# Optimization experiments

Hardware: AMD Instinct MI355X
Metric: run time of the kernel (lower is better)

## Reference

```python
import jax, jax.numpy as jnp
import numpy as np

B = 128          # graphs
N = 512          # nodes per graph
NT = B * N       # total nodes = 65536
E = NT * 16      # total edges = 1048576
IN = 64
H = 128
OUT = 2
L = 4            # num_layers
RATIO = 0.8


def setup_inputs() -> dict:
    key = jax.random.key(0)
    ks = jax.random.split(key, 20)

    def w(k, shape, fan_in):
        return jax.random.normal(k, shape, jnp.float32) / np.sqrt(fan_in)

    x = jax.random.normal(ks[0], (NT, IN), jnp.float32)
    edge_index = jax.random.randint(ks[1], (2, E), 0, NT, dtype=jnp.int32)
    batch = (jnp.arange(NT) // N).astype(jnp.int32)  # equal-size graphs

    return {
        "x": x,
        "edge_index": edge_index,
        "batch": batch,
        # conv1: GraphConv(IN, H, aggr='mean') -> lin_rel (w/ bias) + lin_root (no bias)
        "W1_rel": w(ks[2], (IN, H), IN),
        "W1_root": w(ks[3], (IN, H), IN),
        "b1": jnp.zeros((H,), jnp.float32),
        # convs[0..2]: GraphConv(H, H, aggr='mean'), stacked
        "Wc_rel": w(ks[4], (L - 1, H, H), H),
        "Wc_root": w(ks[5], (L - 1, H, H), H),
        "bc": jnp.zeros((L - 1, H), jnp.float32),
        # SAGPooling score GNN: GraphConv(H, 1) with default aggr='add'
        "pw_rel": w(ks[6], (H,), H),
        "pw_root": w(ks[7], (H,), H),
        "pb": jnp.zeros((1,), jnp.float32),
        # MLP head
        "lin1_W": w(ks[8], (L * H, H), L * H),
        "lin1_b": jnp.zeros((H,), jnp.float32),
        "lin2_W": w(ks[9], (H, OUT), H),
        "lin2_b": jnp.zeros((OUT,), jnp.float32),
    }


def _graph_conv_mean(x, src, dst, emask, W_rel, W_root, b, n):
    # PyG GraphConv: lin_rel(mean_{j->i} x_j) + lin_root(x_i); masked edges excluded.
    msg = x[src] * emask[:, None]                                  # [E, D] gather
    s = jax.ops.segment_sum(msg, dst, num_segments=n)              # [n, D] scatter-add
    cnt = jax.ops.segment_sum(emask, dst, num_segments=n)          # [n]
    agg = s / jnp.maximum(cnt, 1.0)[:, None]                       # zero for isolated nodes
    return agg @ W_rel + x @ W_root + b


def reference(x, edge_index, batch, W1_rel, W1_root, b1, Wc_rel, Wc_root, bc,
              pw_rel, pw_root, pb, lin1_W, lin1_b, lin2_W, lin2_b):
    src = edge_index[0]
    dst = edge_index[1]
    emask = jnp.ones((E,), jnp.float32)
    n = NT
    npg = N  # nodes per graph (all graphs equal size)

    h = jax.nn.relu(_graph_conv_mean(x, src, dst, emask, W1_rel, W1_root, b1, n))
    xs = [h.reshape(B, npg, H).mean(axis=1)]  # global_mean_pool

    for i in range(L - 1):
        h = jax.nn.relu(_graph_conv_mean(h, src, dst, emask, Wc_rel[i], Wc_root[i], bc[i], n))
        xs.append(h.reshape(B, npg, H).mean(axis=1))
        if i % 2 == 0 and i < L - 2:
            # ---- SAGPooling: score via GraphConv(H,1) with add aggregation ----
            smsg = jax.ops.segment_sum(h[src] * emask[:, None], dst, num_segments=n)
            score = smsg @ pw_rel + h @ pw_root + pb[0]            # [n]
            k = int(np.ceil(RATIO * npg))
            topv, topi = jax.lax.top_k(score.reshape(B, npg), k)   # per-graph top-k
            perm = (jnp.arange(B)[:, None] * npg + topi).reshape(-1)  # global kept ids
            h = h[perm] * jnp.tanh(topv.reshape(-1))[:, None]
            # remap edges; edges touching dropped nodes get masked out
            node_map = jnp.full((n,), -1, jnp.int32).at[perm].set(
                jnp.arange(B * k, dtype=jnp.int32))
            ns, nd = node_map[src], node_map[dst]
            keep = ((ns >= 0) & (nd >= 0)).astype(jnp.float32)
            emask = emask * keep
            src = jnp.where(ns >= 0, ns, 0)
            dst = jnp.where(nd >= 0, nd, 0)
            n = B * k
            npg = k

    xcat = jnp.concatenate(xs, axis=-1)                            # JumpingKnowledge 'cat'
    out = jax.nn.relu(xcat @ lin1_W + lin1_b)
    # dropout is identity in eval mode
    out = out @ lin2_W + lin2_b
    return jax.nn.log_softmax(out, axis=-1)
```

## Files before the change

### kernel.cpp

```cpp
#include <hip/hip_runtime.h>
#include <math.h>

#define NT 65536
#define EE 1048576
#define NB 128
#define KK 410
#define HH 128

typedef short bf16x8 __attribute__((ext_vector_type(8)));
typedef float f32x4 __attribute__((ext_vector_type(4)));

__device__ unsigned short g_xb[(size_t)NT * 64];
__device__ unsigned short g_hb1[(size_t)NT * HH];
__device__ unsigned short g_hb2[(size_t)NT * HH];
__device__ unsigned short g_wt1[128 * 128];
__device__ unsigned short g_wtc[3 * 128 * 256];
__device__ unsigned short g_csr1u[EE];
__device__ unsigned short g_keptu[NT];
__device__ unsigned int g_ebuck[EE];
__device__ int g_bcnt[128];
__device__ int g_bcur[128];
__device__ float g_trel[NT];
__device__ float g_troot[NT];
__device__ float g_gatef[NT];
__device__ float g_kinv[NT];
__device__ float g_xc8[4 * NB * 8 * 128];
__device__ int g_rows1[NT + 1];

__device__ __forceinline__ unsigned short* ubuf(int id) {
    switch (id) {
        case 0: return g_xb;
        case 1: return g_hb1;
        case 2: return g_hb2;
        case 3: return g_wt1;
        case 4: return g_wtc;
    }
    return g_xb;
}

__device__ __forceinline__ float b2f(unsigned short u) {
    union { unsigned int i; float f; } v;
    v.i = ((unsigned int)u) << 16;
    return v.f;
}
__device__ __forceinline__ unsigned short f2b(float f) {
    unsigned int x = __float_as_uint(f);
    unsigned int r = x + 0x7fffu + ((x >> 16) & 1u);
    return (unsigned short)(r >> 16);
}
__device__ __forceinline__ bf16x8 scale8(bf16x8 a, float g) {
    bf16x8 r;
#pragma unroll
    for (int i = 0; i < 8; i++) {
        unsigned short u = (unsigned short)a[i];
        r[i] = (short)f2b(b2f(u) * g);
    }
    return r;
}

__global__ __launch_bounds__(256) void k_prep(const float* __restrict__ x,
                                              const float* __restrict__ W1r,
                                              const float* __restrict__ W1o,
                                              const float* __restrict__ Wcr,
                                              const float* __restrict__ Wco,
                                              const int* __restrict__ dst) {
    if (blockIdx.x < 4544) {
        int tid = blockIdx.x * 256 + threadIdx.x;
        if (tid < 1048576) {
            float4 v = *(const float4*)&x[(size_t)tid * 4];
            unsigned int lo = (unsigned int)f2b(v.x) | ((unsigned int)f2b(v.y) << 16);
            unsigned int hi = (unsigned int)f2b(v.z) | ((unsigned int)f2b(v.w) << 16);
            *(uint2*)&g_xb[(size_t)tid * 4] = make_uint2(lo, hi);
        } else if (tid < 1048576 + 16384) {
            int r = tid - 1048576;
            int k = r & 127, n = r >> 7;
            float v = (k < 64) ? W1r[k * 128 + n] : W1o[(k - 64) * 128 + n];
            g_wt1[n * 128 + k] = f2b(v);
        } else {
            int r = tid - (1048576 + 16384);
            int l = r >> 15;
            int k = r & 255, n = (r >> 8) & 127;
            float v = (k < 128) ? Wcr[l * 16384 + k * 128 + n]
                                : Wco[l * 16384 + (k - 128) * 128 + n];
            g_wtc[l * 32768 + n * 256 + k] = f2b(v);
        }
    } else {
        __shared__ int h[128];
        if (threadIdx.x < 128) h[threadIdx.x] = 0;
        __syncthreads();
        int e0 = ((blockIdx.x - 4544) * 256 + threadIdx.x) * 4;
        int4 d = *(const int4*)&dst[e0];
        atomicAdd(&h[d.x >> 9], 1);
        atomicAdd(&h[d.y >> 9], 1);
        atomicAdd(&h[d.z >> 9], 1);
        atomicAdd(&h[d.w >> 9], 1);
        __syncthreads();
        if (threadIdx.x < 128 && h[threadIdx.x]) atomicAdd(&g_bcnt[threadIdx.x], h[threadIdx.x]);
    }
}

__global__ __launch_bounds__(256) void k_bscatter(const int* __restrict__ src,
                                                  const int* __restrict__ dst) {
    __shared__ int h[128];
    __shared__ int base[128];
    __shared__ int sc[128];
    __shared__ int vv[128];
    int t = threadIdx.x;
    if (t < 128) { vv[t] = g_bcnt[t]; sc[t] = vv[t]; h[t] = 0; }
    __syncthreads();
    for (int off = 1; off < 128; off <<= 1) {
        int u = (t >= off && t < 128) ? sc[t - off] : 0;
        __syncthreads();
        if (t < 128) sc[t] += u;
        __syncthreads();
    }
    int e0 = (blockIdx.x * 256 + t) * 4;
    int4 s = *(const int4*)&src[e0];
    int4 d = *(const int4*)&dst[e0];
    int b0 = d.x >> 9, b1 = d.y >> 9, b2 = d.z >> 9, b3 = d.w >> 9;
    atomicAdd(&h[b0], 1);
    atomicAdd(&h[b1], 1);
    atomicAdd(&h[b2], 1);
    atomicAdd(&h[b3], 1);
    __syncthreads();
    if (t < 128) {
        int c = h[t];
        base[t] = (sc[t] - vv[t]) + (c ? atomicAdd(&g_bcur[t], c) : 0);
        h[t] = 0;
    }
    __syncthreads();
    int r0 = atomicAdd(&h[b0], 1);
    g_ebuck[base[b0] + r0] = ((unsigned int)(d.x & 511) << 16) | (unsigned int)s.x;
    int r1 = atomicAdd(&h[b1], 1);
    g_ebuck[base[b1] + r1] = ((unsigned int)(d.y & 511) << 16) | (unsigned int)s.y;
    int r2 = atomicAdd(&h[b2], 1);
    g_ebuck[base[b2] + r2] = ((unsigned int)(d.z & 511) << 16) | (unsigned int)s.z;
    int r3 = atomicAdd(&h[b3], 1);
    g_ebuck[base[b3] + r3] = ((unsigned int)(d.w & 511) << 16) | (unsigned int)s.w;
}

__global__ __launch_bounds__(512) void k_bcsr() {
    __shared__ int hist[512];
    __shared__ int offs[512];
    __shared__ int cur[512];
    __shared__ int sc[128];
    int g = blockIdx.x, t = threadIdx.x;
    if (t < 128) sc[t] = g_bcnt[t];
    hist[t] = 0;
    cur[t] = 0;
    __syncthreads();
    for (int off = 1; off < 128; off <<= 1) {
        int u = (t >= off && t < 128) ? sc[t - off] : 0;
        __syncthreads();
        if (t < 128) sc[t] += u;
        __syncthreads();
    }
    int b0 = sc[g] - g_bcnt[g];
    int b1 = sc[g];
    for (int e = b0 + t; e < b1; e += 512) {
        unsigned int p = g_ebuck[e];
        atomicAdd(&hist[p >> 16], 1);
    }
    __syncthreads();
    int v = hist[t];
    offs[t] = v;
    __syncthreads();
    for (int off = 1; off < 512; off <<= 1) {
        int u = (t >= off) ? offs[t - off] : 0;
        __syncthreads();
        offs[t] += u;
        __syncthreads();
    }
    int excl = offs[t] - v;
    g_rows1[g * 512 + t] = b0 + excl;
    if (t == 511) g_rows1[g * 512 + 512] = b0 + excl + v;
    __syncthreads();
    offs[t] = excl;
    __syncthreads();
    for (int e = b0 + t; e < b1; e += 512) {
        unsigned int p = g_ebuck[e];
        int dl = p >> 16;
        int r = atomicAdd(&cur[dl], 1);
        g_csr1u[b0 + offs[dl] + r] = (unsigned short)(p & 0xFFFFu);
    }
}

template <int KA, int KB, int KC, int GATED, int MASKED, int DOTS, int BGATE>
__global__ __launch_bounds__(256, 4) void k_conv(int hId, int bId, int wId, int wOfs,
                                                 const float* __restrict__ bias, int outId,
                                                 int sec,
                                                 const float* __restrict__ pwr,
                                                 const float* __restrict__ pwt) {
    constexpr int NCHA = KA / 32;
    const int K = KA + KB;
    const unsigned short* h = ubuf(hId);
    const unsigned short* Bp = ubuf(bId);
    const unsigned short* Wt = ubuf(wId) + wOfs;
    unsigned short* out = ubuf(outId);
    __shared__ float s[128];
    int lane = threadIdx.x & 63;
    int w = threadIdx.x >> 6;
    int n16 = lane & 15, quad = lane >> 4;
    int rowbase = blockIdx.x * 64;
    int rowg = rowbase + w * 16;
    int node = rowg + n16;
    if (threadIdx.x < 128) s[threadIdx.x] = 0.f;

    int r0 = g_rows1[node], r1 = g_rows1[node + 1];
    float aggacc[NCHA][8];
#pragma unroll
    for (int ch = 0; ch < NCHA; ch++)
#pragma unroll
        for (int j = 0; j < 8; j++) aggacc[ch][j] = 0.f;
    int kc = 0;
    const unsigned short* hq = h + quad * 8;
#define ACC8(arow, v, gf)                                        \
    arow[0] += gf * b2f((unsigned short)(v.x & 0xffff));         \
    arow[1] += gf * b2f((unsigned short)(v.x >> 16));            \
    arow[2] += gf * b2f((unsigned short)(v.y & 0xffff));         \
    arow[3] += gf * b2f((unsigned short)(v.y >> 16));            \
    arow[4] += gf * b2f((unsigned short)(v.z & 0xffff));         \
    arow[5] += gf * b2f((unsigned short)(v.z >> 16));            \
    arow[6] += gf * b2f((unsigned short)(v.w & 0xffff));         \
    arow[7] += gf * b2f((unsigned short)(v.w >> 16));
    int e = r0;
    for (; e + 2 <= r1; e += 2) {
        int i0 = g_csr1u[e], i1 = g_csr1u[e + 1];
        uint4 v0[NCHA], v1[NCHA];
#pragma unroll
        for (int ch = 0; ch < NCHA; ch++)
            v0[ch] = *(const uint4*)&hq[(size_t)i0 * KA + ch * 32];
#pragma unroll
        for (int ch = 0; ch < NCHA; ch++)
            v1[ch] = *(const uint4*)&hq[(size_t)i1 * KA + ch * 32];
        float gf0 = GATED ? g_gatef[i0] : 1.0f;
        float gf1 = GATED ? g_gatef[i1] : 1.0f;
        if (KC == 1) kc += (int)g_keptu[i0] + (int)g_keptu[i1];
#pragma unroll
        for (int ch = 0; ch < NCHA; ch++) { ACC8(aggacc[ch], v0[ch], gf0) }
#pragma unroll
        for (int ch = 0; ch < NCHA; ch++) { ACC8(aggacc[ch], v1[ch], gf1) }
    }
    if (e < r1) {
        int i0 = g_csr1u[e];
        uint4 v0[NCHA];
#pragma unroll
        for (int ch = 0; ch < NCHA; ch++)
            v0[ch] = *(const uint4*)&hq[(size_t)i0 * KA + ch * 32];
        float gf0 = GATED ? g_gatef[i0] : 1.0f;
        if (KC == 1) kc += (int)g_keptu[i0];
#pragma unroll
        for (int ch = 0; ch < NCHA; ch++) { ACC8(aggacc[ch], v0[ch], gf0) }
    }
#undef ACC8
    float inv;
    if (KC == 0) {
        int c = r1 - r0;
        inv = 1.0f / (float)(c > 0 ? c : 1);
    } else if (KC == 1) {
        inv = 1.0f / (float)(kc > 0 ? kc : 1);
        if (quad == 0) g_kinv[node] = inv;
    } else {
        inv = g_kinv[node];
    }

    bf16x8 afrag[NCHA];
#pragma unroll
    for (int ch = 0; ch < NCHA; ch++)
#pragma unroll
        for (int j = 0; j < 8; j++) afrag[ch][j] = (short)f2b(aggacc[ch][j] * inv);

    float ga = BGATE ? g_gatef[node] : 1.0f;
    f32x4 acc[8];
#pragma unroll
    for (int ct = 0; ct < 8; ct++)
#pragma unroll
        for (int i = 0; i < 4; i++) acc[ct][i] = 0.f;
#pragma unroll
    for (int ks = 0; ks < 8; ks++) {
        if (ks >= K / 32) break;
        bf16x8 a;
        if (ks < NCHA) {
            a = afrag[ks];
        } else {
            int kk = (ks - NCHA) * 32;
            a = *(const bf16x8*)&Bp[(size_t)node * KB + kk + quad * 8];
            if (BGATE) a = scale8(a, ga);
        }
#pragma unroll
        for (int ct = 0; ct < 8; ct++) {
            bf16x8 b = *(const bf16x8*)&Wt[(size_t)(ct * 16 + n16) * K + ks * 32 + quad * 8];
            acc[ct] = __builtin_amdgcn_mfma_f32_16x16x32_bf16(a, b, acc[ct], 0, 0, 0);
        }
    }

    {
        float m[4];
#pragma unroll
        for (int i = 0; i < 4; i++) {
            int r = rowg + quad * 4 + i;
            m[i] = (!MASKED || g_keptu[r]) ? 1.0f : 0.0f;
        }
#pragma unroll
        for (int ct = 0; ct < 8; ct++) {
            int c = ct * 16 + n16;
            float bv = bias[c];
#pragma unroll
            for (int i = 0; i < 4; i++) {
                int r = rowg + quad * 4 + i;
                float v = fmaxf(acc[ct][i] + bv, 0.f) * m[i];
                acc[ct][i] = v;
                out[(size_t)r * 128 + c] = f2b(v);
            }
        }
    }
    __syncthreads();

#pragma unroll
    for (int ct = 0; ct < 8; ct++) {
        float p = acc[ct][0] + acc[ct][1] + acc[ct][2] + acc[ct][3];
        p += __shfl_xor(p, 16);
        p += __shfl_xor(p, 32);
        if (quad == 0) atomicAdd(&s[ct * 16 + n16], p);
    }

    if (DOTS) {
        float pr[8], pt[8];
#pragma unroll
        for (int ct = 0; ct < 8; ct++) {
            pr[ct] = pwr[ct * 16 + n16];
            pt[ct] = pwt[ct * 16 + n16];
        }
#pragma unroll
        for (int i = 0; i < 4; i++) {
            float dr = 0.f, dt = 0.f;
#pragma unroll
            for (int ct = 0; ct < 8; ct++) {
                dr += acc[ct][i] * pr[ct];
                dt += acc[ct][i] * pt[ct];
            }
            dr += __shfl_xor(dr, 1); dt += __shfl_xor(dt, 1);
            dr += __shfl_xor(dr, 2); dt += __shfl_xor(dt, 2);
            dr += __shfl_xor(dr, 4); dt += __shfl_xor(dt, 4);
            dr += __shfl_xor(dr, 8); dt += __shfl_xor(dt, 8);
            if (n16 == 0) {
                int r = rowg + quad * 4 + i;
                g_trel[r] = dr;
                g_troot[r] = dt;
            }
        }
    }
    __syncthreads();
    if (threadIdx.x < 128) {
        int g = blockIdx.x >> 3, e8 = blockIdx.x & 7;
        g_xc8[((sec * NB + g) * 8 + e8) * 128 + threadIdx.x] = s[threadIdx.x];
    }
}

__global__ __launch_bounds__(256) void k_topk(const float* __restrict__ pb) {
    __shared__ float sv[512];
    __shared__ int si[512];
    int g = blockIdx.x, t = threadIdx.x;
    if (t == 0) { g_bcnt[g] = 0; g_bcur[g] = 0; }
    float pbv = pb[0];
    for (int l = t; l < 512; l += 256) {
        int node = g * 512 + l;
        int r0 = g_rows1[node], r1 = g_rows1[node + 1];
        float s = 0.f;
        int e = r0;
        for (; e + 4 <= r1; e += 4) {
            float s0 = g_trel[g_csr1u[e]];
            float s1 = g_trel[g_csr1u[e + 1]];
            float s2 = g_trel[g_csr1u[e + 2]];
            float s3 = g_trel[g_csr1u[e + 3]];
            s += (s0 + s1) + (s2 + s3);
        }
        for (; e < r1; e++) s += g_trel[g_csr1u[e]];
        sv[l] = s + g_troot[node] + pbv;
        si[l] = l;
    }
    __syncthreads();
    for (int k = 2; k <= 512; k <<= 1) {
        for (int j = k >> 1; j > 0; j >>= 1) {
            for (int i = t; i < 512; i += 256) {
                int p = i ^ j;
                if (p > i) {
                    float va = sv[i], vb = sv[p];
                    int ia = si[i], ib = si[p];
                    bool aFirst = (va > vb) || (va == vb && ia < ib);
                    bool up = ((i & k) == 0);
                    if (up != aFirst) { sv[i] = vb; sv[p] = va; si[i] = ib; si[p] = ia; }
                }
            }
            __syncthreads();
        }
    }
    for (int r = t; r < 512; r += 256) {
        int old = g * 512 + si[r];
        if (r < KK) {
            g_gatef[old] = tanhf(sv[r]);
            g_keptu[old] = 1;
        } else {
            g_gatef[old] = 0.f;
            g_keptu[old] = 0;
        }
    }
}

__global__ __launch_bounds__(128) void k_head(const float* __restrict__ W1, const float* __restrict__ b1,
                                              const float* __restrict__ W2, const float* __restrict__ b2,
                                              float* __restrict__ out) {
    __shared__ float xr[512];
    __shared__ float r0[128], r1[128];
    int g = blockIdx.x, t = threadIdx.x;
    for (int i = t; i < 512; i += 128) {
        int sec = i >> 7, c = i & 127;
        const float* p = &g_xc8[((sec * NB + g) * 8) * 128 + c];
        float v = 0.f;
#pragma unroll
        for (int q = 0; q < 8; q++) v += p[q * 128];
        float inv = (sec < 2) ? (1.0f / 512.0f) : (1.0f / 410.0f);
        xr[i] = v * inv;
    }
    __syncthreads();
    float acc = b1[t];
    for (int k = 0; k < 512; k++) acc += xr[k] * W1[k * 128 + t];
    acc = fmaxf(acc, 0.f);
    r0[t] = acc * W2[t * 2 + 0];
    r1[t] = acc * W2[t * 2 + 1];
    __syncthreads();
    for (int off = 64; off > 0; off >>= 1) {
        if (t < off) { r0[t] += r0[t + off]; r1[t] += r1[t + off]; }
        __syncthreads();
    }
    if (t == 0) {
        float z0 = r0[0] + b2[0], z1 = r1[0] + b2[1];
        float m = fmaxf(z0, z1);
        float l = m + logf(expf(z0 - m) + expf(z1 - m));
        out[g * 2 + 0] = z0 - l;
        out[g * 2 + 1] = z1 - l;
    }
}

extern "C" void kernel_launch(void* const* d_in, const int* in_sizes, int n_in,
                              void* d_out, int out_size, void* d_ws, size_t ws_size,
                              hipStream_t stream) {
    const float* x = (const float*)d_in[0];
    const int* ei = (const int*)d_in[1];
    const int* src = ei;
    const int* dst = ei + EE;
    const float* W1r = (const float*)d_in[3];
    const float* W1o = (const float*)d_in[4];
    const float* b1 = (const float*)d_in[5];
    const float* Wcr = (const float*)d_in[6];
    const float* Wco = (const float*)d_in[7];
    const float* bc = (const float*)d_in[8];
    const float* pwr = (const float*)d_in[9];
    const float* pwt = (const float*)d_in[10];
    const float* pb = (const float*)d_in[11];
    const float* l1W = (const float*)d_in[12];
    const float* l1b = (const float*)d_in[13];
    const float* l2W = (const float*)d_in[14];
    const float* l2b = (const float*)d_in[15];
    float* out = (float*)d_out;

    k_prep<<<5568, 256, 0, stream>>>(x, W1r, W1o, Wcr, Wco, dst);

    k_bscatter<<<1024, 256, 0, stream>>>(src, dst);
    k_bcsr<<<128, 512, 0, stream>>>();

    k_conv<64, 64, 0, 0, 0, 0, 0><<<1024, 256, 0, stream>>>(0, 0, 3, 0, b1, 1, 0, pwr, pwt);

    k_conv<128, 128, 0, 0, 0, 1, 0><<<1024, 256, 0, stream>>>(1, 1, 4, 0, bc, 2, 1, pwr, pwt);

    k_topk<<<NB, 256, 0, stream>>>(pb);

    k_conv<128, 128, 1, 1, 1, 0, 1><<<1024, 256, 0, stream>>>(2, 2, 4, 32768, bc + 128, 1, 2, pwr, pwt);

    k_conv<128, 128, 2, 0, 1, 0, 0><<<1024, 256, 0, stream>>>(1, 1, 4, 65536, bc + 256, 2, 3, pwr, pwt);

    k_head<<<NB, 128, 0, stream>>>(l1W, l1b, l2W, l2b, out);
}
```

Before: 511.4 us.

## Split conv edge aggregation and output columns across wave pairs per node tile

Each block now handles 32 nodes with two waves per 16-node group. Each wave aggregates half of a node's edge range, and the halves are combined through shared memory. The MFMA output columns are also split between the two waves, and the grid is doubled with launch bounds raised to 8 blocks. This aims to cut per-thread register pressure and raise occupancy so the latency-bound gather has more parallelism. The cost is extra shared-memory round trips, a bf16 rounding of the partial sum, added barriers, and more per-graph partial pooling slots.

New measurement: 559.8 us. +9.4%, slower.

```diff
diff --git a/kernel.cpp b/kernel.cpp
--- a/kernel.cpp
+++ b/kernel.cpp
@@ -24,7 +24,7 @@
 __device__ float g_troot[NT];
 __device__ float g_gatef[NT];
 __device__ float g_kinv[NT];
-__device__ float g_xc8[4 * NB * 8 * 128];
+__device__ float g_xc16[4 * NB * 16 * 128];
 __device__ int g_rows1[NT + 1];
 
 __device__ __forceinline__ unsigned short* ubuf(int id) {
@@ -186,7 +186,7 @@
 }
 
 template <int KA, int KB, int KC, int GATED, int MASKED, int DOTS, int BGATE>
-__global__ __launch_bounds__(256, 4) void k_conv(int hId, int bId, int wId, int wOfs,
+__global__ __launch_bounds__(256, 8) void k_conv(int hId, int bId, int wId, int wOfs,
                                                  const float* __restrict__ bias, int outId,
                                                  int sec,
                                                  const float* __restrict__ pwr,
@@ -197,16 +197,26 @@
     const unsigned short* Bp = ubuf(bId);
     const unsigned short* Wt = ubuf(wId) + wOfs;
     unsigned short* out = ubuf(outId);
+    __shared__ unsigned short part[2][16][136];
+    __shared__ unsigned short frag[2][16][136];
     __shared__ float s[128];
+    __shared__ float sdr[32], sdt[32];
+    __shared__ int kcs[32];
     int lane = threadIdx.x & 63;
     int w = threadIdx.x >> 6;
+    int g = w >> 1;
+    int h2 = w & 1;
     int n16 = lane & 15, quad = lane >> 4;
-    int rowbase = blockIdx.x * 64;
-    int rowg = rowbase + w * 16;
+    int rowbase = blockIdx.x * 32;
+    int rowg = rowbase + g * 16;
     int node = rowg + n16;
     if (threadIdx.x < 128) s[threadIdx.x] = 0.f;
+    if (threadIdx.x < 32) { sdr[threadIdx.x] = 0.f; sdt[threadIdx.x] = 0.f; }
 
     int r0 = g_rows1[node], r1 = g_rows1[node + 1];
+    int mid = (r0 + r1) >> 1;
+    int ea = h2 ? mid : r0;
+    int eb = h2 ? r1 : mid;
     float aggacc[NCHA][8];
 #pragma unroll
     for (int ch = 0; ch < NCHA; ch++)
@@ -223,8 +233,8 @@
     arow[5] += gf * b2f((unsigned short)(v.z >> 16));            \
     arow[6] += gf * b2f((unsigned short)(v.w & 0xffff));         \
     arow[7] += gf * b2f((unsigned short)(v.w >> 16));
-    int e = r0;
-    for (; e + 2 <= r1; e += 2) {
+    int e = ea;
+    for (; e + 2 <= eb; e += 2) {
         int i0 = g_csr1u[e], i1 = g_csr1u[e + 1];
         uint4 v0[NCHA], v1[NCHA];
 #pragma unroll
@@ -241,7 +251,7 @@
 #pragma unroll
         for (int ch = 0; ch < NCHA; ch++) { ACC8(aggacc[ch], v1[ch], gf1) }
     }
-    if (e < r1) {
+    if (e < eb) {
         int i0 = g_csr1u[e];
         uint4 v0[NCHA];
 #pragma unroll
@@ -253,44 +263,68 @@
         for (int ch = 0; ch < NCHA; ch++) { ACC8(aggacc[ch], v0[ch], gf0) }
     }
 #undef ACC8
-    float inv;
-    if (KC == 0) {
-        int c = r1 - r0;
-        inv = 1.0f / (float)(c > 0 ? c : 1);
-    } else if (KC == 1) {
-        inv = 1.0f / (float)(kc > 0 ? kc : 1);
-        if (quad == 0) g_kinv[node] = inv;
-    } else {
-        inv = g_kinv[node];
-    }
-
-    bf16x8 afrag[NCHA];
-#pragma unroll
-    for (int ch = 0; ch < NCHA; ch++)
-#pragma unroll
-        for (int j = 0; j < 8; j++) afrag[ch][j] = (short)f2b(aggacc[ch][j] * inv);
+
+    if (h2 == 0) {
+#pragma unroll
+        for (int ch = 0; ch < NCHA; ch++) {
+            bf16x8 pk;
+#pragma unroll
+            for (int j = 0; j < 8; j++) pk[j] = (short)f2b(aggacc[ch][j]);
+            *(bf16x8*)&part[g][n16][ch * 32 + quad * 8] = pk;
+        }
+        if (KC == 1 && quad == 0) kcs[g * 16 + n16] = kc;
+    }
+    __syncthreads();
+
+    if (h2 == 1) {
+#pragma unroll
+        for (int ch = 0; ch < NCHA; ch++) {
+            bf16x8 pv = *(const bf16x8*)&part[g][n16][ch * 32 + quad * 8];
+#pragma unroll
+            for (int j = 0; j < 8; j++) aggacc[ch][j] += b2f((unsigned short)pv[j]);
+        }
+        float inv;
+        if (KC == 0) {
+            int c = r1 - r0;
+            inv = 1.0f / (float)(c > 0 ? c : 1);
+        } else if (KC == 1) {
+            kc += kcs[g * 16 + n16];
+            inv = 1.0f / (float)(kc > 0 ? kc : 1);
+            if (quad == 0) g_kinv[node] = inv;
+        } else {
+            inv = g_kinv[node];
+        }
+#pragma unroll
+        for (int ch = 0; ch < NCHA; ch++) {
+            bf16x8 fk;
+#pragma unroll
+            for (int j = 0; j < 8; j++) fk[j] = (short)f2b(aggacc[ch][j] * inv);
+            *(bf16x8*)&frag[g][n16][ch * 32 + quad * 8] = fk;
+        }
+    }
+    __syncthreads();
 
     float ga = BGATE ? g_gatef[node] : 1.0f;
-    f32x4 acc[8];
-#pragma unroll
-    for (int ct = 0; ct < 8; ct++)
-#pragma unroll
-        for (int i = 0; i < 4; i++) acc[ct][i] = 0.f;
-#pragma unroll
-    for (int ks = 0; ks < 8; ks++) {
-        if (ks >= K / 32) break;
+    f32x4 acc[4];
+#pragma unroll
+    for (int c4 = 0; c4 < 4; c4++)
+#pragma unroll
+        for (int i = 0; i < 4; i++) acc[c4][i] = 0.f;
+#pragma unroll
+    for (int ks = 0; ks < K / 32; ks++) {
         bf16x8 a;
         if (ks < NCHA) {
-            a = afrag[ks];
+            a = *(const bf16x8*)&frag[g][n16][ks * 32 + quad * 8];
         } else {
             int kk = (ks - NCHA) * 32;
             a = *(const bf16x8*)&Bp[(size_t)node * KB + kk + quad * 8];
             if (BGATE) a = scale8(a, ga);
         }
 #pragma unroll
-        for (int ct = 0; ct < 8; ct++) {
+        for (int c4 = 0; c4 < 4; c4++) {
+            int ct = h2 * 4 + c4;
             bf16x8 b = *(const bf16x8*)&Wt[(size_t)(ct * 16 + n16) * K + ks * 32 + quad * 8];
-            acc[ct] = __builtin_amdgcn_mfma_f32_16x16x32_bf16(a, b, acc[ct], 0, 0, 0);
+            acc[c4] = __builtin_amdgcn_mfma_f32_16x16x32_bf16(a, b, acc[c4], 0, 0, 0);
         }
     }
 
@@ -302,58 +336,60 @@
             m[i] = (!MASKED || g_keptu[r]) ? 1.0f : 0.0f;
         }
 #pragma unroll
-        for (int ct = 0; ct < 8; ct++) {
-            int c = ct * 16 + n16;
+        for (int c4 = 0; c4 < 4; c4++) {
+            int c = (h2 * 4 + c4) * 16 + n16;
             float bv = bias[c];
 #pragma unroll
             for (int i = 0; i < 4; i++) {
                 int r = rowg + quad * 4 + i;
-                float v = fmaxf(acc[ct][i] + bv, 0.f) * m[i];
-                acc[ct][i] = v;
+                float v = fmaxf(acc[c4][i] + bv, 0.f) * m[i];
+                acc[c4][i] = v;
                 out[(size_t)r * 128 + c] = f2b(v);
             }
         }
     }
-    __syncthreads();
-
-#pragma unroll
-    for (int ct = 0; ct < 8; ct++) {
-        float p = acc[ct][0] + acc[ct][1] + acc[ct][2] + acc[ct][3];
+
+#pragma unroll
+    for (int c4 = 0; c4 < 4; c4++) {
+        float p = acc[c4][0] + acc[c4][1] + acc[c4][2] + acc[c4][3];
         p += __shfl_xor(p, 16);
         p += __shfl_xor(p, 32);
-        if (quad == 0) atomicAdd(&s[ct * 16 + n16], p);
+        if (quad == 0) atomicAdd(&s[(h2 * 4 + c4) * 16 + n16], p);
     }
 
     if (DOTS) {
-        float pr[8], pt[8];
-#pragma unroll
-        for (int ct = 0; ct < 8; ct++) {
-            pr[ct] = pwr[ct * 16 + n16];
-            pt[ct] = pwt[ct * 16 + n16];
+        float pr[4], pt[4];
+#pragma unroll
+        for (int c4 = 0; c4 < 4; c4++) {
+            pr[c4] = pwr[(h2 * 4 + c4) * 16 + n16];
+            pt[c4] = pwt[(h2 * 4 + c4) * 16 + n16];
         }
 #pragma unroll
         for (int i = 0; i < 4; i++) {
             float dr = 0.f, dt = 0.f;
 #pragma unroll
-            for (int ct = 0; ct < 8; ct++) {
-                dr += acc[ct][i] * pr[ct];
-                dt += acc[ct][i] * pt[ct];
+            for (int c4 = 0; c4 < 4; c4++) {
+                dr += acc[c4][i] * pr[c4];
+                dt += acc[c4][i] * pt[c4];
             }
             dr += __shfl_xor(dr, 1); dt += __shfl_xor(dt, 1);
             dr += __shfl_xor(dr, 2); dt += __shfl_xor(dt, 2);
             dr += __shfl_xor(dr, 4); dt += __shfl_xor(dt, 4);
             dr += __shfl_xor(dr, 8); dt += __shfl_xor(dt, 8);
             if (n16 == 0) {
-                int r = rowg + quad * 4 + i;
-                g_trel[r] = dr;
-                g_troot[r] = dt;
+                atomicAdd(&sdr[g * 16 + quad * 4 + i], dr);
+                atomicAdd(&sdt[g * 16 + quad * 4 + i], dt);
             }
         }
     }
     __syncthreads();
     if (threadIdx.x < 128) {
-        int g = blockIdx.x >> 3, e8 = blockIdx.x & 7;
-        g_xc8[((sec * NB + g) * 8 + e8) * 128 + threadIdx.x] = s[threadIdx.x];
+        int gr = blockIdx.x >> 4, e16 = blockIdx.x & 15;
+        g_xc16[((sec * NB + gr) * 16 + e16) * 128 + threadIdx.x] = s[threadIdx.x];
+    }
+    if (DOTS && threadIdx.x < 32) {
+        g_trel[rowbase + threadIdx.x] = sdr[threadIdx.x];
+        g_troot[rowbase + threadIdx.x] = sdt[threadIdx.x];
     }
 }
 
@@ -415,10 +451,10 @@
     int g = blockIdx.x, t = threadIdx.x;
     for (int i = t; i < 512; i += 128) {
         int sec = i >> 7, c = i & 127;
-        const float* p = &g_xc8[((sec * NB + g) * 8) * 128 + c];
+        const float* p = &g_xc16[((sec * NB + g) * 16) * 128 + c];
         float v = 0.f;
 #pragma unroll
-        for (int q = 0; q < 8; q++) v += p[q * 128];
+        for (int q = 0; q < 16; q++) v += p[q * 128];
         float inv = (sec < 2) ? (1.0f / 512.0f) : (1.0f / 410.0f);
         xr[i] = v * inv;
     }
@@ -469,15 +505,15 @@
     k_bscatter<<<1024, 256, 0, stream>>>(src, dst);
     k_bcsr<<<128, 512, 0, stream>>>();
 
-    k_conv<64, 64, 0, 0, 0, 0, 0><<<1024, 256, 0, stream>>>(0, 0, 3, 0, b1, 1, 0, pwr, pwt);
-
-    k_conv<128, 128, 0, 0, 0, 1, 0><<<1024, 256, 0, stream>>>(1, 1, 4, 0, bc, 2, 1, pwr, pwt);
+    k_conv<64, 64, 0, 0, 0, 0, 0><<<2048, 256, 0, stream>>>(0, 0, 3, 0, b1, 1, 0, pwr, pwt);
+
+    k_conv<128, 128, 0, 0, 0, 1, 0><<<2048, 256, 0, stream>>>(1, 1, 4, 0, bc, 2, 1, pwr, pwt);
 
     k_topk<<<NB, 256, 0, stream>>>(pb);
 
-    k_conv<128, 128, 1, 1, 1, 0, 1><<<1024, 256, 0, stream>>>(2, 2, 4, 32768, bc + 128, 1, 2, pwr, pwt);
-
-    k_conv<128, 128, 2, 0, 1, 0, 0><<<1024, 256, 0, stream>>>(1, 1, 4, 65536, bc + 256, 2, 3, pwr, pwt);
+    k_conv<128, 128, 1, 1, 1, 0, 1><<<2048, 256, 0, stream>>>(2, 2, 4, 32768, bc + 128, 1, 2, pwr, pwt);
+
+    k_conv<128, 128, 2, 0, 1, 0, 0><<<2048, 256, 0, stream>>>(1, 1, 4, 65536, bc + 256, 2, 3, pwr, pwt);
 
     k_head<<<NB, 128, 0, stream>>>(l1W, l1b, l2W, l2b, out);
 }
```
